# Kernel optimization log

Hardware: AMD Instinct MI355X
Metric: run time of the kernel (lower is better)

The kernel has to match this reference:

```python
import jax, jax.numpy as jnp
import numpy as np
from jax import lax

B_, N, C, NH, KB = 4096, 64, 192, 6, 8
WH = WW = 8  # win_size
HD = C // NH
KS = 5  # depthwise kernel size (distance=2)


def _rel_pos_index(wh, ww, k_bound):
    ch = np.arange(wh); cw = np.arange(ww)
    coords = np.stack(np.meshgrid(ch, cw, indexing='ij'))  # (2, wh, ww)
    cf = coords.reshape(2, -1)
    rel = cf[:, :, None] - cf[:, None, :]
    rel = np.clip(rel, -(k_bound - 1), k_bound - 1).transpose(1, 2, 0).astype(np.int32)
    rel[..., 0] += k_bound - 1
    rel[..., 1] += k_bound - 1
    rel[..., 0] *= 2 * k_bound - 1
    return rel.sum(-1)  # (N, N) indices into (2k-1)^2 table


def setup_inputs() -> dict:
    key = jax.random.key(0)
    ks = jax.random.split(key, 12)
    s = 0.02
    x = jax.random.normal(ks[0], (B_, N, C), dtype=jnp.float32)
    wq = jax.random.normal(ks[1], (C, C), dtype=jnp.float32) * s
    bq = jnp.zeros((C,), dtype=jnp.float32)
    wkv = jax.random.normal(ks[2], (C, 3 * C), dtype=jnp.float32) * s
    bkv = jnp.zeros((3 * C,), dtype=jnp.float32)
    rpb_table = jax.random.normal(ks[3], ((2 * KB - 1) * (2 * KB - 1), NH), dtype=jnp.float32) * s
    rel_index = jnp.asarray(_rel_pos_index(WH, WW, KB), dtype=jnp.int32)
    dw_w = jax.random.normal(ks[4], (C, 1, KS, KS), dtype=jnp.float32) * s   # depthwise, groups=C
    dw_b = jnp.zeros((C,), dtype=jnp.float32)
    pw_w = jax.random.normal(ks[5], (C, C // NH, 1, 1), dtype=jnp.float32) * s  # 1x1, groups=NH
    pw_b = jnp.zeros((C,), dtype=jnp.float32)
    proj_w = jax.random.normal(ks[6], (C, C), dtype=jnp.float32) * s
    proj_b = jnp.zeros((C,), dtype=jnp.float32)
    return dict(x=x, wq=wq, bq=bq, wkv=wkv, bkv=bkv, rpb_table=rpb_table,
                rel_index=rel_index, dw_w=dw_w, dw_b=dw_b, pw_w=pw_w, pw_b=pw_b,
                proj_w=proj_w, proj_b=proj_b)


def reference(x, wq, bq, wkv, bkv, rpb_table, rel_index, dw_w, dw_b, pw_w, pw_b, proj_w, proj_b):
    B, Nn, Cc = x.shape
    H = int(round(Nn ** 0.5))
    scale = (Cc // NH) ** -0.5
    # QKV projections
    q = (x @ wq + bq).reshape(B, Nn, NH, HD).transpose(0, 2, 1, 3)          # (B, nH, N, hd)
    kv = (x @ wkv + bkv).reshape(B, Nn, 3, NH, HD)
    k = kv[:, :, 0].transpose(0, 2, 1, 3)                                    # (B, nH, N, hd)
    v = kv[:, :, 1].transpose(0, 2, 1, 3)                                    # (B, nH, N, hd)
    v_r = kv[:, :, 2].transpose(0, 2, 3, 1).reshape(B, Cc, H, H)             # (B, C, H, H)
    # attention scores + relative position bias
    attn = jnp.einsum('bhnd,bhmd->bhnm', q * scale, k)
    bias = rpb_table[rel_index.reshape(-1)].reshape(Nn, Nn, NH).transpose(2, 0, 1)  # (nH, N, N)
    attn = jax.nn.softmax(attn + bias[None], axis=-1)
    # positional conv branch: depthwise 5x5 then grouped 1x1
    dn = ('NCHW', 'OIHW', 'NCHW')
    p = lax.conv_general_dilated(v_r, dw_w, (1, 1), 'SAME', dimension_numbers=dn,
                                 feature_group_count=Cc) + dw_b[None, :, None, None]
    p = lax.conv_general_dilated(p, pw_w, (1, 1), 'SAME', dimension_numbers=dn,
                                 feature_group_count=NH) + pw_b[None, :, None, None]
    position = p.reshape(B, Cc, Nn).transpose(0, 2, 1)                       # (B, N, C)
    out = jnp.einsum('bhnm,bhmd->bnhd', attn, v).reshape(B, Nn, Cc) + position
    return out @ proj_w + proj_b
```

## Files before the change

### kernel.cpp

```cpp
#include <hip/hip_runtime.h>

typedef _Float16 half8 __attribute__((ext_vector_type(8)));
typedef _Float16 half4 __attribute__((ext_vector_type(4)));
typedef _Float16 half2 __attribute__((ext_vector_type(2)));
typedef float floatx4 __attribute__((ext_vector_type(4)));

union H8 { half8 h8; half2 h2[4]; int i[4]; };


__global__ __launch_bounds__(512) void prep_kernel(
    const float* __restrict__ wq, const float* __restrict__ wkv,
    const float* __restrict__ proj_w, const float* __restrict__ rpb,
    const int* __restrict__ rel,
    const float* __restrict__ dw_w, const float* __restrict__ dw_b,
    const float* __restrict__ pw_w,
    _Float16* __restrict__ WtF, _Float16* __restrict__ PtF,
    float* __restrict__ biasF, _Float16* __restrict__ dwF,
    _Float16* __restrict__ dwbF, _Float16* __restrict__ pwF)
{
    int idx = blockIdx.x * 512 + threadIdx.x;
    if (idx < 147456) {
        int j = idx & 7, lane = (idx >> 3) & 63, t = idx >> 9;
        int ks = t % 6, nt = t / 6;
        int k = ks * 32 + (lane >> 4) * 8 + j;
        int n = nt * 16 + (lane & 15);
        float v = (n < 192) ? wq[k * 192 + n] : wkv[k * 576 + (n - 192)];
        WtF[idx] = (_Float16)v;
    } else if (idx < 184320) {
        int i2 = idx - 147456;
        int j = i2 & 7, lane = (i2 >> 3) & 63, t = i2 >> 9;
        int ks = t % 6, nt = t / 6;
        int k = ks * 32 + (lane >> 4) * 8 + j;
        int n = nt * 16 + (lane & 15);
        PtF[i2] = (_Float16)proj_w[k * 192 + n];
    } else if (idx < 208896) {
        int i2 = idx - 184320;
        int r = i2 & 3, lane = (i2 >> 2) & 63, t = i2 >> 8;
        int ntq = t & 3, mt = (t >> 2) & 3, h = t >> 4;
        int m = mt * 16 + (lane >> 4) * 4 + r;
        int n = ntq * 16 + (lane & 15);
        biasF[i2] = rpb[rel[n * 64 + m] * 6 + h];
    } else if (idx < 213696) {
        int i2 = idx - 208896;
        int j = i2 & 7, t = i2 >> 3;
        int tap = t % 25, gk = t / 25;
        int c = (gk >> 2) * 32 + (gk & 3) * 8 + j;
        dwF[i2] = (_Float16)dw_w[c * 25 + tap];
    } else if (idx < 213888) {
        int i2 = idx - 213696;
        int j = i2 & 7, gk = i2 >> 3;
        int c = (gk >> 2) * 32 + (gk & 3) * 8 + j;
        dwbF[i2] = (_Float16)dw_b[c];
    } else if (idx < 220032) {
        int i2 = idx - 213888;
        int j = i2 & 7, lane = (i2 >> 3) & 63, t = i2 >> 9;
        int ntc = t & 1, g = t >> 1;
        int oc = g * 32 + ntc * 16 + (lane & 15);
        int ic = (lane >> 4) * 8 + j;
        pwF[i2] = (_Float16)pw_w[oc * 32 + ic];
    }
}


#define XO   0
#define QO   12800
#define KO   28160
#define VTO  43520
#define VRO  57344
#define ZO   70144

__global__ __launch_bounds__(512, 2) void wa_main(
    const float* __restrict__ xg,
    const float* __restrict__ bq, const float* __restrict__ bkv,
    const float* __restrict__ proj_bg, const float* __restrict__ pw_b,
    const _Float16* __restrict__ WtF, const _Float16* __restrict__ PtF,
    const float* __restrict__ biasF,
    const _Float16* __restrict__ dwF, const _Float16* __restrict__ dwbF,
    const _Float16* __restrict__ pwF,
    float* __restrict__ outg)
{
    extern __shared__ unsigned char smem[];
    _Float16* sHalf = (_Float16*)smem;
    float* sBias = (float*)(smem + 140304);
    float* sOut32 = (float*)(smem + 25600);

    const int b    = blockIdx.x;
    const int tid  = threadIdx.x;
    const int lane = tid & 63;
    const int wv   = tid >> 6;
    const int mrow = lane & 15;
    const int kq   = lane >> 4;
    const float scale = 0.17677669529663687f;

    const float* xb = xg + (size_t)b * 12288;
    #pragma unroll
    for (int it = 0; it < 6; ++it) {
        int f4  = it * 512 + tid;
        int row = f4 / 48;
        int col = (f4 % 48) * 4;
        float4 v = ((const float4*)xb)[f4];
        _Float16* dst = sHalf + XO + row * 200 + col;
        dst[0] = (_Float16)v.x; dst[1] = (_Float16)v.y;
        dst[2] = (_Float16)v.z; dst[3] = (_Float16)v.w;
    }
    for (int idx = tid; idx < 960; idx += 512) {
        float v;
        if      (idx < 192) v = bq[idx];
        else if (idx < 768) v = bkv[idx - 192];
        else                v = proj_bg[idx - 768];
        sBias[idx] = v;
    }
    if (tid < 8) sHalf[ZO + tid] = (_Float16)0.0f;
    __syncthreads();

    {
        half8 af[4][6];
        #pragma unroll
        for (int mt = 0; mt < 4; ++mt)
            #pragma unroll
            for (int ks = 0; ks < 6; ++ks)
                af[mt][ks] = *(const half8*)(sHalf + XO + (mt * 16 + mrow) * 200 + ks * 32 + kq * 8);

        #pragma unroll 1
        for (int it = 0; it < 6; ++it) {
            int nt   = it * 8 + wv;
            int ncol = nt * 16 + mrow;
            half8 bf[6];
            #pragma unroll
            for (int ks = 0; ks < 6; ++ks)
                bf[ks] = ((const half8*)WtF)[(nt * 6 + ks) * 64 + lane];
            float bv = sBias[ncol];
            #pragma unroll
            for (int mt = 0; mt < 4; ++mt) {
                floatx4 acc = {bv, bv, bv, bv};
                #pragma unroll
                for (int ks = 0; ks < 6; ++ks)
                    acc = __builtin_amdgcn_mfma_f32_16x16x32_f16(af[mt][ks], bf[ks], acc, 0, 0, 0);
                int m0 = mt * 16 + kq * 4;
                if (nt < 12) {
                    int h = ncol >> 5, d = ncol & 31;
                    _Float16* q = sHalf + QO + (h * 64 + m0) * 40 + d;
                    #pragma unroll
                    for (int r = 0; r < 4; ++r) q[r * 40] = (_Float16)(acc[r] * scale);
                } else if (nt < 24) {
                    int cc = ncol - 192; int h = cc >> 5, d = cc & 31;
                    _Float16* kk = sHalf + KO + (h * 64 + m0) * 40 + d;
                    #pragma unroll
                    for (int r = 0; r < 4; ++r) kk[r * 40] = (_Float16)acc[r];
                } else if (nt < 36) {
                    int cc = ncol - 384; int h = cc >> 5, d = cc & 31;
                    half4 p;
                    #pragma unroll
                    for (int r = 0; r < 4; ++r) p[r] = (_Float16)acc[r];
                    *(half4*)(sHalf + VTO + (h * 32 + d) * 72 + m0) = p;
                } else {
                    int c = ncol - 576;
                    #pragma unroll
                    for (int r = 0; r < 4; ++r)
                        sHalf[VRO + (m0 + r) * 200 + c] = (_Float16)acc[r];
                }
            }
        }
    }
    __syncthreads();

    if (wv < 6) {
        const int h = wv;

        const int cb32 = h * 32 + kq * 8;
        const half8* dwFp = (const half8*)dwF + (h * 4 + kq) * 25;
        H8 bini; bini.h8 = ((const half8*)dwbF)[h * 4 + kq];
        half2 cacc[4][4];
        #pragma unroll
        for (int mt = 0; mt < 4; ++mt)
            #pragma unroll
            for (int p = 0; p < 4; ++p) cacc[mt][p] = bini.h2[p];

        int ni[4], nj[4];
        #pragma unroll
        for (int mt = 0; mt < 4; ++mt) { int n = mt * 16 + mrow; ni[mt] = n >> 3; nj[mt] = n & 7; }

        #pragma unroll 5
        for (int t = 0; t < 25; ++t) {
            H8 w; w.h8 = dwFp[t];
            int di = t / 5 - 2, dj = t % 5 - 2;
            #pragma unroll
            for (int mt = 0; mt < 4; ++mt) {
                int ii = ni[mt] + di, jj = nj[mt] + dj;
                bool ok = ((unsigned)ii < 8u) & ((unsigned)jj < 8u);
                int off = ok ? (VRO + ((ii << 3) + jj) * 200 + cb32) : ZO;
                H8 d; d.h8 = *(const half8*)(sHalf + off);
                #pragma unroll
                for (int p = 0; p < 4; ++p) cacc[mt][p] += d.h2[p] * w.h2[p];
            }
        }
        half8 dwA[4];
        #pragma unroll
        for (int mt = 0; mt < 4; ++mt) {
            H8 u;
            #pragma unroll
            for (int p = 0; p < 4; ++p) u.h2[p] = cacc[mt][p];
            dwA[mt] = u.h8;
        }

        floatx4 accPV[4][2];
        #pragma unroll
        for (int ntc = 0; ntc < 2; ++ntc) {
            half8 pwB = ((const half8*)pwF)[(h * 2 + ntc) * 64 + lane];
            float pb = pw_b[h * 32 + ntc * 16 + mrow];
            #pragma unroll
            for (int mt = 0; mt < 4; ++mt) {
                floatx4 acc = {pb, pb, pb, pb};
                accPV[mt][ntc] = __builtin_amdgcn_mfma_f32_16x16x32_f16(dwA[mt], pwB, acc, 0, 0, 0);
            }
        }

        half8 aK[4], bQ[4];
        #pragma unroll
        for (int t4 = 0; t4 < 4; ++t4) {
            aK[t4] = *(const half8*)(sHalf + KO + (h * 64 + t4 * 16 + mrow) * 40 + kq * 8);
            bQ[t4] = *(const half8*)(sHalf + QO + (h * 64 + t4 * 16 + mrow) * 40 + kq * 8);
        }
        floatx4 st[4][4];
        #pragma unroll
        for (int mtk = 0; mtk < 4; ++mtk)
            #pragma unroll
            for (int ntq = 0; ntq < 4; ++ntq) {
                floatx4 bb = *(const floatx4*)(biasF + (((h * 4 + mtk) * 4 + ntq) * 64 + lane) * 4);
                st[mtk][ntq] = __builtin_amdgcn_mfma_f32_16x16x32_f16(aK[mtk], bQ[ntq], bb, 0, 0, 0);
            }

        #pragma unroll
        for (int ntq = 0; ntq < 4; ++ntq) {
            float mx = st[0][ntq][0];
            #pragma unroll
            for (int mtk = 0; mtk < 4; ++mtk)
                #pragma unroll
                for (int r = 0; r < 4; ++r) mx = fmaxf(mx, st[mtk][ntq][r]);
            mx = fmaxf(mx, __shfl_xor(mx, 16));
            mx = fmaxf(mx, __shfl_xor(mx, 32));
            float sm = 0.0f;
            #pragma unroll
            for (int mtk = 0; mtk < 4; ++mtk)
                #pragma unroll
                for (int r = 0; r < 4; ++r) {
                    float e = __expf(st[mtk][ntq][r] - mx);
                    st[mtk][ntq][r] = e;
                    sm += e;
                }
            sm += __shfl_xor(sm, 16);
            sm += __shfl_xor(sm, 32);
            float inv = 1.0f / sm;
            #pragma unroll
            for (int mtk = 0; mtk < 4; ++mtk)
                #pragma unroll
                for (int r = 0; r < 4; ++r) st[mtk][ntq][r] *= inv;
        }

        int pk[4][4][2];
        #pragma unroll
        for (int mtk = 0; mtk < 4; ++mtk)
            #pragma unroll
            for (int ntq = 0; ntq < 4; ++ntq) {
                union { _Float16 hh[2]; int ii; } u0, u1;
                u0.hh[0] = (_Float16)st[mtk][ntq][0]; u0.hh[1] = (_Float16)st[mtk][ntq][1];
                u1.hh[0] = (_Float16)st[mtk][ntq][2]; u1.hh[1] = (_Float16)st[mtk][ntq][3];
                pk[mtk][ntq][0] = u0.ii;
                pk[mtk][ntq][1] = u1.ii;
            }
        const int idxA = ((kq & 1) * 32 + mrow) * 4;
        const int idxB = idxA + 64;
        const bool sel = (kq >= 2);
        half8 aP[4][2];
        #pragma unroll
        for (int ks = 0; ks < 2; ++ks)
            #pragma unroll
            for (int mtq = 0; mtq < 4; ++mtq) {
                int s0 = ks * 2, s1 = ks * 2 + 1;
                int a0 = __builtin_amdgcn_ds_bpermute(idxA, pk[s0][mtq][0]);
                int b0 = __builtin_amdgcn_ds_bpermute(idxA, pk[s1][mtq][0]);
                int a1 = __builtin_amdgcn_ds_bpermute(idxA, pk[s0][mtq][1]);
                int b1 = __builtin_amdgcn_ds_bpermute(idxA, pk[s1][mtq][1]);
                int a2 = __builtin_amdgcn_ds_bpermute(idxB, pk[s0][mtq][0]);
                int b2 = __builtin_amdgcn_ds_bpermute(idxB, pk[s1][mtq][0]);
                int a3 = __builtin_amdgcn_ds_bpermute(idxB, pk[s0][mtq][1]);
                int b3 = __builtin_amdgcn_ds_bpermute(idxB, pk[s1][mtq][1]);
                H8 u;
                u.i[0] = sel ? b0 : a0;
                u.i[1] = sel ? b1 : a1;
                u.i[2] = sel ? b2 : a2;
                u.i[3] = sel ? b3 : a3;
                aP[mtq][ks] = u.h8;
            }

        half8 bV[2][2];
        #pragma unroll
        for (int ntd = 0; ntd < 2; ++ntd)
            #pragma unroll
            for (int ks = 0; ks < 2; ++ks)
                bV[ntd][ks] = *(const half8*)(sHalf + VTO + (h * 32 + ntd * 16 + mrow) * 72 + ks * 32 + kq * 8);
        #pragma unroll
        for (int mtq = 0; mtq < 4; ++mtq)
            #pragma unroll
            for (int ntd = 0; ntd < 2; ++ntd) {
                floatx4 o = accPV[mtq][ntd];
                o = __builtin_amdgcn_mfma_f32_16x16x32_f16(aP[mtq][0], bV[ntd][0], o, 0, 0, 0);
                o = __builtin_amdgcn_mfma_f32_16x16x32_f16(aP[mtq][1], bV[ntd][1], o, 0, 0, 0);
                int c = h * 32 + ntd * 16 + mrow;
                #pragma unroll
                for (int r = 0; r < 4; ++r)
                    sHalf[VRO + (mtq * 16 + kq * 4 + r) * 200 + c] = (_Float16)o[r];
            }
    }
    __syncthreads();

    {
        int mt = wv >> 1;
        half8 af[6];
        #pragma unroll
        for (int ks = 0; ks < 6; ++ks)
            af[ks] = *(const half8*)(sHalf + VRO + (mt * 16 + mrow) * 200 + ks * 32 + kq * 8);
        #pragma unroll 1
        for (int it = 0; it < 6; ++it) {
            int nt = (wv & 1) * 6 + it;
            int ncol = nt * 16 + mrow;
            half8 bf[6];
            #pragma unroll
            for (int ks = 0; ks < 6; ++ks)
                bf[ks] = ((const half8*)PtF)[(nt * 6 + ks) * 64 + lane];
            float bv = sBias[768 + ncol];
            floatx4 acc = {bv, bv, bv, bv};
            #pragma unroll
            for (int ks = 0; ks < 6; ++ks)
                acc = __builtin_amdgcn_mfma_f32_16x16x32_f16(af[ks], bf[ks], acc, 0, 0, 0);
            int m0 = mt * 16 + kq * 4;
            #pragma unroll
            for (int r = 0; r < 4; ++r)
                sOut32[(m0 + r) * 196 + ncol] = acc[r];
        }
    }
    __syncthreads();

    {
        float* og = outg + (size_t)b * 12288;
        #pragma unroll
        for (int it = 0; it < 6; ++it) {
            int f = it * 2048 + tid * 4;
            int n = f / 192;
            int c = f - n * 192;
            float4 v = *(const float4*)(sOut32 + n * 196 + c);
            *(float4*)(og + f) = v;
        }
    }
}

extern "C" void kernel_launch(void* const* d_in, const int* in_sizes, int n_in,
                              void* d_out, int out_size, void* d_ws, size_t ws_size,
                              hipStream_t stream) {
    (void)in_sizes; (void)n_in; (void)out_size; (void)ws_size;
    const float* x      = (const float*)d_in[0];
    const float* wq     = (const float*)d_in[1];
    const float* bq     = (const float*)d_in[2];
    const float* wkv    = (const float*)d_in[3];
    const float* bkv    = (const float*)d_in[4];
    const float* rpb    = (const float*)d_in[5];
    const int*   rel    = (const int*)d_in[6];
    const float* dw_w   = (const float*)d_in[7];
    const float* dw_b   = (const float*)d_in[8];
    const float* pw_w   = (const float*)d_in[9];
    const float* pw_b   = (const float*)d_in[10];
    const float* proj_w = (const float*)d_in[11];
    const float* proj_b = (const float*)d_in[12];

    _Float16* WtF  = (_Float16*)d_ws;
    _Float16* PtF  = (_Float16*)((char*)d_ws + 294912);
    float*    biasF= (float*)((char*)d_ws + 368640);
    _Float16* dwF  = (_Float16*)((char*)d_ws + 466944);
    _Float16* dwbF = (_Float16*)((char*)d_ws + 476544);
    _Float16* pwF  = (_Float16*)((char*)d_ws + 476928);

    prep_kernel<<<430, 512, 0, stream>>>(wq, wkv, proj_w, rpb, rel, dw_w, dw_b, pw_w,
                                         WtF, PtF, biasF, dwF, dwbF, pwF);
    wa_main<<<4096, 512, 144144, stream>>>(x, bq, bkv, proj_b, pw_b,
                                           WtF, PtF, biasF, dwF, dwbF, pwF,
                                           (float*)d_out);
}
```

Measured before the change: 606.6 us.

## Keep per-head Q/K/V in registers, shrink LDS and use 384-thread blocks

Restructures the fused window-attention kernel so each of six waves computes the Q, K and V projection tiles for its own head and keeps them packed in registers. It then redistributes those tiles with ds_bpermute instead of staging Q, K and V^T in shared memory. The LDS footprint drops from about 144KB to about 55KB and blocks shrink to 384 threads, so three blocks can be resident per CU instead of two. It also streams A operands from LDS per MFMA, processes the softmax in two halves to limit register pressure, and writes the projection output directly to global memory, which removes the staging buffer and one barrier. The risks are higher register pressure, extra bpermute traffic, and uncoalesced strided global stores in the final projection.

```diff
diff --git a/kernel.cpp b/kernel.cpp
--- a/kernel.cpp
+++ b/kernel.cpp
@@ -5,7 +5,31 @@
 typedef _Float16 half2 __attribute__((ext_vector_type(2)));
 typedef float floatx4 __attribute__((ext_vector_type(4)));
 
-union H8 { half8 h8; half2 h2[4]; int i[4]; };
+union H8 { half8 h8; half4 h4[2]; half2 h2[4]; int i[4]; };
+
+__device__ __forceinline__ int packh2(float a, float b) {
+    union { _Float16 h[2]; int i; } u;
+    u.h[0] = (_Float16)a; u.h[1] = (_Float16)b;
+    return u.i;
+}
+
+__device__ __forceinline__ half8 gather8(int idxA, int idxB, bool sel,
+                                         int A0, int A1, int B0, int B1) {
+    int a0 = __builtin_amdgcn_ds_bpermute(idxA, A0);
+    int b0 = __builtin_amdgcn_ds_bpermute(idxA, B0);
+    int a1 = __builtin_amdgcn_ds_bpermute(idxA, A1);
+    int b1 = __builtin_amdgcn_ds_bpermute(idxA, B1);
+    int a2 = __builtin_amdgcn_ds_bpermute(idxB, A0);
+    int b2 = __builtin_amdgcn_ds_bpermute(idxB, B0);
+    int a3 = __builtin_amdgcn_ds_bpermute(idxB, A1);
+    int b3 = __builtin_amdgcn_ds_bpermute(idxB, B1);
+    H8 u;
+    u.i[0] = sel ? b0 : a0;
+    u.i[1] = sel ? b1 : a1;
+    u.i[2] = sel ? b2 : a2;
+    u.i[3] = sel ? b3 : a3;
+    return u.h8;
+}
 
 
 __global__ __launch_bounds__(512) void prep_kernel(
@@ -63,13 +87,10 @@
 
 
 #define XO   0
-#define QO   12800
-#define KO   28160
-#define VTO  43520
-#define VRO  57344
-#define ZO   70144
-
-__global__ __launch_bounds__(512, 2) void wa_main(
+#define VRO  12800
+#define ZO   25600
+
+__global__ __launch_bounds__(384, 3) void wa_main(
     const float* __restrict__ xg,
     const float* __restrict__ bq, const float* __restrict__ bkv,
     const float* __restrict__ proj_bg, const float* __restrict__ pw_b,
@@ -81,29 +102,29 @@
 {
     extern __shared__ unsigned char smem[];
     _Float16* sHalf = (_Float16*)smem;
-    float* sBias = (float*)(smem + 140304);
-    float* sOut32 = (float*)(smem + 25600);
+    float* sBias = (float*)(smem + 51216);
 
     const int b    = blockIdx.x;
     const int tid  = threadIdx.x;
     const int lane = tid & 63;
-    const int wv   = tid >> 6;
+    const int h    = tid >> 6;
     const int mrow = lane & 15;
     const int kq   = lane >> 4;
     const float scale = 0.17677669529663687f;
 
     const float* xb = xg + (size_t)b * 12288;
     #pragma unroll
-    for (int it = 0; it < 6; ++it) {
-        int f4  = it * 512 + tid;
+    for (int it = 0; it < 8; ++it) {
+        int f4  = it * 384 + tid;
         int row = f4 / 48;
         int col = (f4 % 48) * 4;
         float4 v = ((const float4*)xb)[f4];
-        _Float16* dst = sHalf + XO + row * 200 + col;
-        dst[0] = (_Float16)v.x; dst[1] = (_Float16)v.y;
-        dst[2] = (_Float16)v.z; dst[3] = (_Float16)v.w;
-    }
-    for (int idx = tid; idx < 960; idx += 512) {
+        half4 p;
+        p[0] = (_Float16)v.x; p[1] = (_Float16)v.y;
+        p[2] = (_Float16)v.z; p[3] = (_Float16)v.w;
+        *(half4*)(sHalf + XO + row * 200 + col) = p;
+    }
+    for (int idx = tid; idx < 960; idx += 384) {
         float v;
         if      (idx < 192) v = bq[idx];
         else if (idx < 768) v = bkv[idx - 192];
@@ -113,130 +134,173 @@
     if (tid < 8) sHalf[ZO + tid] = (_Float16)0.0f;
     __syncthreads();
 
-    {
-        half8 af[4][6];
-        #pragma unroll
-        for (int mt = 0; mt < 4; ++mt)
-            #pragma unroll
-            for (int ks = 0; ks < 6; ++ks)
-                af[mt][ks] = *(const half8*)(sHalf + XO + (mt * 16 + mrow) * 200 + ks * 32 + kq * 8);
-
-        #pragma unroll 1
-        for (int it = 0; it < 6; ++it) {
-            int nt   = it * 8 + wv;
-            int ncol = nt * 16 + mrow;
+    int qst[2][4][2], kst[2][4][2], vst[2][4][2];
+
+    #pragma unroll
+    for (int qk = 0; qk < 2; ++qk) {
+        #pragma unroll
+        for (int t = 0; t < 2; ++t) {
+            int nt = qk * 12 + 2 * h + t;
             half8 bf[6];
             #pragma unroll
             for (int ks = 0; ks < 6; ++ks)
                 bf[ks] = ((const half8*)WtF)[(nt * 6 + ks) * 64 + lane];
-            float bv = sBias[ncol];
-            #pragma unroll
-            for (int mt = 0; mt < 4; ++mt) {
-                floatx4 acc = {bv, bv, bv, bv};
+            floatx4 binit = *(const floatx4*)(sBias + nt * 16 + kq * 4);
+            #pragma unroll
+            for (int mt4 = 0; mt4 < 4; ++mt4) {
+                floatx4 acc = binit;
                 #pragma unroll
-                for (int ks = 0; ks < 6; ++ks)
-                    acc = __builtin_amdgcn_mfma_f32_16x16x32_f16(af[mt][ks], bf[ks], acc, 0, 0, 0);
-                int m0 = mt * 16 + kq * 4;
-                if (nt < 12) {
-                    int h = ncol >> 5, d = ncol & 31;
-                    _Float16* q = sHalf + QO + (h * 64 + m0) * 40 + d;
-                    #pragma unroll
-                    for (int r = 0; r < 4; ++r) q[r * 40] = (_Float16)(acc[r] * scale);
-                } else if (nt < 24) {
-                    int cc = ncol - 192; int h = cc >> 5, d = cc & 31;
-                    _Float16* kk = sHalf + KO + (h * 64 + m0) * 40 + d;
-                    #pragma unroll
-                    for (int r = 0; r < 4; ++r) kk[r * 40] = (_Float16)acc[r];
-                } else if (nt < 36) {
-                    int cc = ncol - 384; int h = cc >> 5, d = cc & 31;
-                    half4 p;
-                    #pragma unroll
-                    for (int r = 0; r < 4; ++r) p[r] = (_Float16)acc[r];
-                    *(half4*)(sHalf + VTO + (h * 32 + d) * 72 + m0) = p;
+                for (int ks = 0; ks < 6; ++ks) {
+                    half8 af = *(const half8*)(sHalf + XO + (mt4 * 16 + mrow) * 200 + ks * 32 + kq * 8);
+                    acc = __builtin_amdgcn_mfma_f32_16x16x32_f16(bf[ks], af, acc, 0, 0, 0);
+                }
+                if (qk == 0) {
+                    qst[t][mt4][0] = packh2(acc[0] * scale, acc[1] * scale);
+                    qst[t][mt4][1] = packh2(acc[2] * scale, acc[3] * scale);
                 } else {
-                    int c = ncol - 576;
-                    #pragma unroll
-                    for (int r = 0; r < 4; ++r)
-                        sHalf[VRO + (m0 + r) * 200 + c] = (_Float16)acc[r];
+                    kst[t][mt4][0] = packh2(acc[0], acc[1]);
+                    kst[t][mt4][1] = packh2(acc[2], acc[3]);
                 }
             }
         }
     }
-    __syncthreads();
-
-    if (wv < 6) {
-        const int h = wv;
-
-        const int cb32 = h * 32 + kq * 8;
-        const half8* dwFp = (const half8*)dwF + (h * 4 + kq) * 25;
-        H8 bini; bini.h8 = ((const half8*)dwbF)[h * 4 + kq];
-        half2 cacc[4][4];
-        #pragma unroll
-        for (int mt = 0; mt < 4; ++mt)
-            #pragma unroll
-            for (int p = 0; p < 4; ++p) cacc[mt][p] = bini.h2[p];
-
-        int ni[4], nj[4];
-        #pragma unroll
-        for (int mt = 0; mt < 4; ++mt) { int n = mt * 16 + mrow; ni[mt] = n >> 3; nj[mt] = n & 7; }
-
-        #pragma unroll 5
-        for (int t = 0; t < 25; ++t) {
-            H8 w; w.h8 = dwFp[t];
-            int di = t / 5 - 2, dj = t % 5 - 2;
-            #pragma unroll
-            for (int mt = 0; mt < 4; ++mt) {
-                int ii = ni[mt] + di, jj = nj[mt] + dj;
-                bool ok = ((unsigned)ii < 8u) & ((unsigned)jj < 8u);
-                int off = ok ? (VRO + ((ii << 3) + jj) * 200 + cb32) : ZO;
-                H8 d; d.h8 = *(const half8*)(sHalf + off);
-                #pragma unroll
-                for (int p = 0; p < 4; ++p) cacc[mt][p] += d.h2[p] * w.h2[p];
-            }
-        }
-        half8 dwA[4];
+
+    #pragma unroll
+    for (int t = 0; t < 2; ++t) {
+        int nt = 24 + 2 * h + t;
+        half8 bf[6];
+        #pragma unroll
+        for (int ks = 0; ks < 6; ++ks)
+            bf[ks] = ((const half8*)WtF)[(nt * 6 + ks) * 64 + lane];
+        float bv = sBias[nt * 16 + mrow];
         #pragma unroll
         for (int mt = 0; mt < 4; ++mt) {
-            H8 u;
-            #pragma unroll
-            for (int p = 0; p < 4; ++p) u.h2[p] = cacc[mt][p];
-            dwA[mt] = u.h8;
-        }
-
-        floatx4 accPV[4][2];
-        #pragma unroll
-        for (int ntc = 0; ntc < 2; ++ntc) {
-            half8 pwB = ((const half8*)pwF)[(h * 2 + ntc) * 64 + lane];
-            float pb = pw_b[h * 32 + ntc * 16 + mrow];
-            #pragma unroll
-            for (int mt = 0; mt < 4; ++mt) {
-                floatx4 acc = {pb, pb, pb, pb};
-                accPV[mt][ntc] = __builtin_amdgcn_mfma_f32_16x16x32_f16(dwA[mt], pwB, acc, 0, 0, 0);
-            }
-        }
-
-        half8 aK[4], bQ[4];
-        #pragma unroll
-        for (int t4 = 0; t4 < 4; ++t4) {
-            aK[t4] = *(const half8*)(sHalf + KO + (h * 64 + t4 * 16 + mrow) * 40 + kq * 8);
-            bQ[t4] = *(const half8*)(sHalf + QO + (h * 64 + t4 * 16 + mrow) * 40 + kq * 8);
-        }
-        floatx4 st[4][4];
+            floatx4 acc = {bv, bv, bv, bv};
+            #pragma unroll
+            for (int ks = 0; ks < 6; ++ks) {
+                half8 af = *(const half8*)(sHalf + XO + (mt * 16 + mrow) * 200 + ks * 32 + kq * 8);
+                acc = __builtin_amdgcn_mfma_f32_16x16x32_f16(af, bf[ks], acc, 0, 0, 0);
+            }
+            vst[t][mt][0] = packh2(acc[0], acc[1]);
+            vst[t][mt][1] = packh2(acc[2], acc[3]);
+        }
+    }
+
+    #pragma unroll
+    for (int t = 0; t < 2; ++t) {
+        int nt = 36 + 2 * h + t;
+        half8 bf[6];
+        #pragma unroll
+        for (int ks = 0; ks < 6; ++ks)
+            bf[ks] = ((const half8*)WtF)[(nt * 6 + ks) * 64 + lane];
+        floatx4 binit = *(const floatx4*)(sBias + nt * 16 + kq * 4);
+        #pragma unroll
+        for (int mt4 = 0; mt4 < 4; ++mt4) {
+            floatx4 acc = binit;
+            #pragma unroll
+            for (int ks = 0; ks < 6; ++ks) {
+                half8 af = *(const half8*)(sHalf + XO + (mt4 * 16 + mrow) * 200 + ks * 32 + kq * 8);
+                acc = __builtin_amdgcn_mfma_f32_16x16x32_f16(bf[ks], af, acc, 0, 0, 0);
+            }
+            union { int i2[2]; half4 h4; } u;
+            u.i2[0] = packh2(acc[0], acc[1]);
+            u.i2[1] = packh2(acc[2], acc[3]);
+            *(half4*)(sHalf + VRO + (mt4 * 16 + mrow) * 200 + 32 * h + 16 * t + kq * 4) = u.h4;
+        }
+    }
+
+    const int cb32 = h * 32 + kq * 8;
+    const half8* dwFp = (const half8*)dwF + (h * 4 + kq) * 25;
+    H8 bini; bini.h8 = ((const half8*)dwbF)[h * 4 + kq];
+    half2 cacc[4][4];
+    #pragma unroll
+    for (int mt = 0; mt < 4; ++mt)
+        #pragma unroll
+        for (int p = 0; p < 4; ++p) cacc[mt][p] = bini.h2[p];
+
+    int ni[4], nj[4];
+    #pragma unroll
+    for (int mt = 0; mt < 4; ++mt) { int n = mt * 16 + mrow; ni[mt] = n >> 3; nj[mt] = n & 7; }
+
+    #pragma unroll 5
+    for (int t = 0; t < 25; ++t) {
+        H8 w; w.h8 = dwFp[t];
+        int di = t / 5 - 2, dj = t % 5 - 2;
+        #pragma unroll
+        for (int mt = 0; mt < 4; ++mt) {
+            int ii = ni[mt] + di, jj = nj[mt] + dj;
+            bool ok = ((unsigned)ii < 8u) & ((unsigned)jj < 8u);
+            int off = ok ? (VRO + ((ii << 3) + jj) * 200 + cb32) : ZO;
+            H8 d; d.h8 = *(const half8*)(sHalf + off);
+            #pragma unroll
+            for (int p = 0; p < 4; ++p) cacc[mt][p] += d.h2[p] * w.h2[p];
+        }
+    }
+    half8 dwA[4];
+    #pragma unroll
+    for (int mt = 0; mt < 4; ++mt) {
+        H8 u;
+        #pragma unroll
+        for (int p = 0; p < 4; ++p) u.h2[p] = cacc[mt][p];
+        dwA[mt] = u.h8;
+    }
+
+    floatx4 accPV[4][2];
+    #pragma unroll
+    for (int ntc = 0; ntc < 2; ++ntc) {
+        half8 pwB = ((const half8*)pwF)[(h * 2 + ntc) * 64 + lane];
+        float4 pb4 = *(const float4*)(pw_b + h * 32 + ntc * 16 + kq * 4);
+        #pragma unroll
+        for (int mt = 0; mt < 4; ++mt) {
+            floatx4 acc = {pb4.x, pb4.y, pb4.z, pb4.w};
+            accPV[mt][ntc] = __builtin_amdgcn_mfma_f32_16x16x32_f16(pwB, dwA[mt], acc, 0, 0, 0);
+        }
+    }
+
+    const int idxA = ((kq & 1) * 32 + mrow) * 4;
+    const int idxB = idxA + 64;
+    const bool sel = (kq >= 2);
+
+    half8 aK[4];
+    #pragma unroll
+    for (int mtk = 0; mtk < 4; ++mtk)
+        aK[mtk] = gather8(idxA, idxB, sel,
+                          kst[0][mtk][0], kst[0][mtk][1],
+                          kst[1][mtk][0], kst[1][mtk][1]);
+    half8 bV[2][2];
+    #pragma unroll
+    for (int ntd = 0; ntd < 2; ++ntd)
+        #pragma unroll
+        for (int ks2 = 0; ks2 < 2; ++ks2)
+            bV[ntd][ks2] = gather8(idxA, idxB, sel,
+                                   vst[ntd][2 * ks2][0],     vst[ntd][2 * ks2][1],
+                                   vst[ntd][2 * ks2 + 1][0], vst[ntd][2 * ks2 + 1][1]);
+
+    #pragma unroll
+    for (int hf = 0; hf < 2; ++hf) {
+        half8 bQ[2];
+        #pragma unroll
+        for (int q2 = 0; q2 < 2; ++q2)
+            bQ[q2] = gather8(idxA, idxB, sel,
+                             qst[0][hf * 2 + q2][0], qst[0][hf * 2 + q2][1],
+                             qst[1][hf * 2 + q2][0], qst[1][hf * 2 + q2][1]);
+
+        floatx4 stt[4][2];
         #pragma unroll
         for (int mtk = 0; mtk < 4; ++mtk)
             #pragma unroll
-            for (int ntq = 0; ntq < 4; ++ntq) {
-                floatx4 bb = *(const floatx4*)(biasF + (((h * 4 + mtk) * 4 + ntq) * 64 + lane) * 4);
-                st[mtk][ntq] = __builtin_amdgcn_mfma_f32_16x16x32_f16(aK[mtk], bQ[ntq], bb, 0, 0, 0);
-            }
-
-        #pragma unroll
-        for (int ntq = 0; ntq < 4; ++ntq) {
-            float mx = st[0][ntq][0];
+            for (int q2 = 0; q2 < 2; ++q2) {
+                floatx4 bb = *(const floatx4*)(biasF + (((h * 4 + mtk) * 4 + hf * 2 + q2) * 64 + lane) * 4);
+                stt[mtk][q2] = __builtin_amdgcn_mfma_f32_16x16x32_f16(aK[mtk], bQ[q2], bb, 0, 0, 0);
+            }
+
+        #pragma unroll
+        for (int q2 = 0; q2 < 2; ++q2) {
+            float mx = stt[0][q2][0];
             #pragma unroll
             for (int mtk = 0; mtk < 4; ++mtk)
                 #pragma unroll
-                for (int r = 0; r < 4; ++r) mx = fmaxf(mx, st[mtk][ntq][r]);
+                for (int r = 0; r < 4; ++r) mx = fmaxf(mx, stt[mtk][q2][r]);
             mx = fmaxf(mx, __shfl_xor(mx, 16));
             mx = fmaxf(mx, __shfl_xor(mx, 32));
             float sm = 0.0f;
@@ -244,8 +308,8 @@
             for (int mtk = 0; mtk < 4; ++mtk)
                 #pragma unroll
                 for (int r = 0; r < 4; ++r) {
-                    float e = __expf(st[mtk][ntq][r] - mx);
-                    st[mtk][ntq][r] = e;
+                    float e = __expf(stt[mtk][q2][r] - mx);
+                    stt[mtk][q2][r] = e;
                     sm += e;
                 }
             sm += __shfl_xor(sm, 16);
@@ -254,102 +318,66 @@
             #pragma unroll
             for (int mtk = 0; mtk < 4; ++mtk)
                 #pragma unroll
-                for (int r = 0; r < 4; ++r) st[mtk][ntq][r] *= inv;
-        }
-
-        int pk[4][4][2];
+                for (int r = 0; r < 4; ++r) stt[mtk][q2][r] *= inv;
+        }
+
+        int pk[4][2][2];
         #pragma unroll
         for (int mtk = 0; mtk < 4; ++mtk)
             #pragma unroll
-            for (int ntq = 0; ntq < 4; ++ntq) {
-                union { _Float16 hh[2]; int ii; } u0, u1;
-                u0.hh[0] = (_Float16)st[mtk][ntq][0]; u0.hh[1] = (_Float16)st[mtk][ntq][1];
-                u1.hh[0] = (_Float16)st[mtk][ntq][2]; u1.hh[1] = (_Float16)st[mtk][ntq][3];
-                pk[mtk][ntq][0] = u0.ii;
-                pk[mtk][ntq][1] = u1.ii;
-            }
-        const int idxA = ((kq & 1) * 32 + mrow) * 4;
-        const int idxB = idxA + 64;
-        const bool sel = (kq >= 2);
-        half8 aP[4][2];
-        #pragma unroll
-        for (int ks = 0; ks < 2; ++ks)
-            #pragma unroll
-            for (int mtq = 0; mtq < 4; ++mtq) {
-                int s0 = ks * 2, s1 = ks * 2 + 1;
-                int a0 = __builtin_amdgcn_ds_bpermute(idxA, pk[s0][mtq][0]);
-                int b0 = __builtin_amdgcn_ds_bpermute(idxA, pk[s1][mtq][0]);
-                int a1 = __builtin_amdgcn_ds_bpermute(idxA, pk[s0][mtq][1]);
-                int b1 = __builtin_amdgcn_ds_bpermute(idxA, pk[s1][mtq][1]);
-                int a2 = __builtin_amdgcn_ds_bpermute(idxB, pk[s0][mtq][0]);
-                int b2 = __builtin_amdgcn_ds_bpermute(idxB, pk[s1][mtq][0]);
-                int a3 = __builtin_amdgcn_ds_bpermute(idxB, pk[s0][mtq][1]);
-                int b3 = __builtin_amdgcn_ds_bpermute(idxB, pk[s1][mtq][1]);
-                H8 u;
-                u.i[0] = sel ? b0 : a0;
-                u.i[1] = sel ? b1 : a1;
-                u.i[2] = sel ? b2 : a2;
-                u.i[3] = sel ? b3 : a3;
-                aP[mtq][ks] = u.h8;
-            }
-
-        half8 bV[2][2];
-        #pragma unroll
-        for (int ntd = 0; ntd < 2; ++ntd)
-            #pragma unroll
-            for (int ks = 0; ks < 2; ++ks)
-                bV[ntd][ks] = *(const half8*)(sHalf + VTO + (h * 32 + ntd * 16 + mrow) * 72 + ks * 32 + kq * 8);
-        #pragma unroll
-        for (int mtq = 0; mtq < 4; ++mtq)
-            #pragma unroll
-            for (int ntd = 0; ntd < 2; ++ntd) {
-                floatx4 o = accPV[mtq][ntd];
-                o = __builtin_amdgcn_mfma_f32_16x16x32_f16(aP[mtq][0], bV[ntd][0], o, 0, 0, 0);
-                o = __builtin_amdgcn_mfma_f32_16x16x32_f16(aP[mtq][1], bV[ntd][1], o, 0, 0, 0);
-                int c = h * 32 + ntd * 16 + mrow;
+            for (int q2 = 0; q2 < 2; ++q2) {
+                pk[mtk][q2][0] = packh2(stt[mtk][q2][0], stt[mtk][q2][1]);
+                pk[mtk][q2][1] = packh2(stt[mtk][q2][2], stt[mtk][q2][3]);
+            }
+        #pragma unroll
+        for (int q2 = 0; q2 < 2; ++q2) {
+            int mtq = hf * 2 + q2;
+            #pragma unroll
+            for (int ks2 = 0; ks2 < 2; ++ks2) {
+                half8 aP = gather8(idxA, idxB, sel,
+                                   pk[2 * ks2][q2][0],     pk[2 * ks2][q2][1],
+                                   pk[2 * ks2 + 1][q2][0], pk[2 * ks2 + 1][q2][1]);
                 #pragma unroll
-                for (int r = 0; r < 4; ++r)
-                    sHalf[VRO + (mtq * 16 + kq * 4 + r) * 200 + c] = (_Float16)o[r];
-            }
-    }
+                for (int ntd = 0; ntd < 2; ++ntd)
+                    accPV[mtq][ntd] = __builtin_amdgcn_mfma_f32_16x16x32_f16(
+                        bV[ntd][ks2], aP, accPV[mtq][ntd], 0, 0, 0);
+            }
+        }
+    }
+
+    #pragma unroll
+    for (int mtq = 0; mtq < 4; ++mtq)
+        #pragma unroll
+        for (int ntd = 0; ntd < 2; ++ntd) {
+            floatx4 o = accPV[mtq][ntd];
+            union { int i2[2]; half4 h4; } u;
+            u.i2[0] = packh2(o[0], o[1]);
+            u.i2[1] = packh2(o[2], o[3]);
+            *(half4*)(sHalf + VRO + (mtq * 16 + mrow) * 200 + h * 32 + ntd * 16 + kq * 4) = u.h4;
+        }
     __syncthreads();
 
-    {
-        int mt = wv >> 1;
-        half8 af[6];
+    float* og = outg + (size_t)b * 12288;
+    #pragma unroll
+    for (int tnt = 0; tnt < 2; ++tnt) {
+        int nt = 2 * h + tnt;
+        half8 bf[6];
         #pragma unroll
         for (int ks = 0; ks < 6; ++ks)
-            af[ks] = *(const half8*)(sHalf + VRO + (mt * 16 + mrow) * 200 + ks * 32 + kq * 8);
-        #pragma unroll 1
-        for (int it = 0; it < 6; ++it) {
-            int nt = (wv & 1) * 6 + it;
-            int ncol = nt * 16 + mrow;
-            half8 bf[6];
-            #pragma unroll
-            for (int ks = 0; ks < 6; ++ks)
-                bf[ks] = ((const half8*)PtF)[(nt * 6 + ks) * 64 + lane];
-            float bv = sBias[768 + ncol];
+            bf[ks] = ((const half8*)PtF)[(nt * 6 + ks) * 64 + lane];
+        float bv = sBias[768 + nt * 16 + mrow];
+        #pragma unroll
+        for (int mt = 0; mt < 4; ++mt) {
             floatx4 acc = {bv, bv, bv, bv};
             #pragma unroll
-            for (int ks = 0; ks < 6; ++ks)
-                acc = __builtin_amdgcn_mfma_f32_16x16x32_f16(af[ks], bf[ks], acc, 0, 0, 0);
+            for (int ks = 0; ks < 6; ++ks) {
+                half8 af = *(const half8*)(sHalf + VRO + (mt * 16 + mrow) * 200 + ks * 32 + kq * 8);
+                acc = __builtin_amdgcn_mfma_f32_16x16x32_f16(af, bf[ks], acc, 0, 0, 0);
+            }
             int m0 = mt * 16 + kq * 4;
             #pragma unroll
             for (int r = 0; r < 4; ++r)
-                sOut32[(m0 + r) * 196 + ncol] = acc[r];
-        }
-    }
-    __syncthreads();
-
-    {
-        float* og = outg + (size_t)b * 12288;
-        #pragma unroll
-        for (int it = 0; it < 6; ++it) {
-            int f = it * 2048 + tid * 4;
-            int n = f / 192;
-            int c = f - n * 192;
-            float4 v = *(const float4*)(sOut32 + n * 196 + c);
-            *(float4*)(og + f) = v;
+                og[(m0 + r) * 192 + nt * 16 + mrow] = acc[r];
         }
     }
 }
@@ -381,7 +409,7 @@
 
     prep_kernel<<<430, 512, 0, stream>>>(wq, wkv, proj_w, rpb, rel, dw_w, dw_b, pw_w,
                                          WtF, PtF, biasF, dwF, dwbF, pwF);
-    wa_main<<<4096, 512, 144144, stream>>>(x, bq, bkv, proj_b, pw_b,
-                                           WtF, PtF, biasF, dwF, dwbF, pwF,
-                                           (float*)d_out);
+    wa_main<<<4096, 384, 55056, stream>>>(x, bq, bkv, proj_b, pw_b,
+                                          WtF, PtF, biasF, dwF, dwbF, pwF,
+                                          (float*)d_out);
 }
```

Result: slower. 789.5 us (+30.1%).
